# Kernel tuning notes

Hardware: AMD Instinct MI355X
Metric: run time of the kernel (lower is better)

The kernel has to match this reference:

```python
import jax, jax.numpy as jnp
import numpy as np

N, L, H, D = 4, 1024, 8, 64

def setup_inputs() -> dict:
    key = jax.random.key(0)
    ks = jax.random.split(key, 6)
    names = ["q_real", "q_imag", "k_real", "k_imag", "v_real", "v_imag"]
    return {n: jax.random.normal(k, (N, L, H, D), dtype=jnp.float32) for n, k in zip(names, ks)}


def reference(q_real, q_imag, k_real, k_imag, v_real, v_imag):
    d = q_real.shape[-1]
    scale = 1.0 / np.sqrt(d).astype(np.float32)
    # complex QK^T: (ar+i*ai)(br+i*bi) -> 4 real einsums, scores shape (N,H,L,S)
    s_real = (jnp.einsum('nlhd,nshd->nhls', q_real, k_real)
              - jnp.einsum('nlhd,nshd->nhls', q_imag, k_imag))
    s_imag = (jnp.einsum('nlhd,nshd->nhls', q_real, k_imag)
              + jnp.einsum('nlhd,nshd->nhls', q_imag, k_real))
    # complex softmax = independent softmax on real and imag parts
    w_real = jax.nn.softmax(scale * s_real, axis=-1)
    w_imag = jax.nn.softmax(scale * s_imag, axis=-1)
    # complex_dropout on complex input is identity (original code drops nothing)
    # complex AV
    u_real = (jnp.einsum('nhls,nshd->nlhd', w_real, v_real)
              - jnp.einsum('nhls,nshd->nlhd', w_imag, v_imag))
    u_imag = (jnp.einsum('nhls,nshd->nlhd', w_real, v_imag)
              + jnp.einsum('nhls,nshd->nlhd', w_imag, v_real))
    # attn_weights.permute(0,2,1,3).mean(dim=-2): (N,H,L,S)->(N,L,H,S), mean over H -> (N,L,S)
    a_real = w_real.mean(axis=1)
    a_imag = w_imag.mean(axis=1)
    return (u_real, u_imag, a_real, a_imag)
```

## Files before the change

kernel.cpp:

```cpp
#include <hip/hip_runtime.h>

#define N_ 4
#define L_ 1024
#define H_ 8
#define D_ 64

typedef _Float16 f16x8 __attribute__((ext_vector_type(8)));
typedef _Float16 f16x4 __attribute__((ext_vector_type(4)));
typedef _Float16 f16x2 __attribute__((ext_vector_type(2)));
typedef float f32x4 __attribute__((ext_vector_type(4)));

#define MFMA(A, B, C) __builtin_amdgcn_mfma_f32_16x16x32_f16(A, B, C, 0, 0, 0)

__device__ __forceinline__ ushort f2h(float x) {
    union { _Float16 h; ushort u; } c;
    c.h = (_Float16)x;
    return c.u;
}
__device__ __forceinline__ f16x8 ld8(const ushort* p) {
    return *(const f16x8*)p;
}
__device__ __forceinline__ f16x4 pack4(float a, float b, float c, float d) {
    union { f16x4 v; f16x2 h[2]; } u;
    u.h[0] = __builtin_bit_cast(f16x2, __builtin_amdgcn_cvt_pkrtz(a, b));
    u.h[1] = __builtin_bit_cast(f16x2, __builtin_amdgcn_cvt_pkrtz(c, d));
    return u.v;
}
__device__ __forceinline__ f16x8 negf(f16x8 a) {
    uint4 u = __builtin_bit_cast(uint4, a);
    u.x ^= 0x80008000u; u.y ^= 0x80008000u; u.z ^= 0x80008000u; u.w ^= 0x80008000u;
    return __builtin_bit_cast(f16x8, u);
}
__device__ __forceinline__ f16x8 cvt8s(const float* p, float s) {
    float4 a = *(const float4*)p;
    float4 b = *(const float4*)(p + 4);
    union { f16x8 v; _Float16 e[8]; } u;
    u.e[0] = (_Float16)(a.x * s); u.e[1] = (_Float16)(a.y * s);
    u.e[2] = (_Float16)(a.z * s); u.e[3] = (_Float16)(a.w * s);
    u.e[4] = (_Float16)(b.x * s); u.e[5] = (_Float16)(b.y * s);
    u.e[6] = (_Float16)(b.z * s); u.e[7] = (_Float16)(b.w * s);
    return u.v;
}
#define SCQ 0.18033688011112f
__device__ __forceinline__ f16x8 cvt8(const float* p) { return cvt8s(p, SCQ); }

__device__ __forceinline__ void gl_lds16(const ushort* g, ushort* l) {
    __builtin_amdgcn_global_load_lds(
        (const __attribute__((address_space(1))) unsigned int*)g,
        (__attribute__((address_space(3))) unsigned int*)l, 16, 0, 0);
}

__global__ void cvt_k(const float* __restrict__ k_r, const float* __restrict__ k_i,
                      ushort* __restrict__ dst) {
    int gid = blockIdx.x * 256 + threadIdx.x;
    int aid = gid >> 19;
    int idx = (gid & 0x7FFFF) << 2;
    int d  = idx & 63;
    int l  = (idx >> 6) & 1023;
    int hh = (idx >> 16) & 7;
    int n  = idx >> 19;
    const float* src = aid ? k_i : k_r;
    const float4 v = *(const float4*)(src + (((long)n * 1024 + l) * 8 + hh) * 64 + d);
    ushort4 o = make_ushort4(f2h(v.x), f2h(v.y), f2h(v.z), f2h(v.w));
    *(ushort4*)(dst + ((long)aid << 21) + idx) = o;
}

__global__ void cvt_v(const float* __restrict__ vr, const float* __restrict__ vi,
                      ushort* __restrict__ dst) {
    __shared__ ushort t[64][72];
    int bid = blockIdx.x;
    int aid = bid >> 9;
    int b   = bid & 511;
    int s0  = (b & 15) << 6;
    int hh  = (b >> 4) & 7;
    int n   = b >> 7;
    const float* src = aid ? vi : vr;
    int tid = threadIdx.x;
    int r  = tid >> 4;
    int cq = (tid & 15) << 2;
#pragma unroll
    for (int it = 0; it < 4; ++it) {
        int s = s0 + it * 16 + r;
        const float4 v = *(const float4*)(src + (((long)n * 1024 + s) * 8 + hh) * 64 + cq);
        t[it * 16 + r][cq + 0] = f2h(v.x);
        t[it * 16 + r][cq + 1] = f2h(v.y);
        t[it * 16 + r][cq + 2] = f2h(v.z);
        t[it * 16 + r][cq + 3] = f2h(v.w);
    }
    __syncthreads();
    const int rem = cq & 31;
    const int noff = (cq & 32) + (((rem & 15) >> 2) << 3) + ((rem >> 4) << 2);
#pragma unroll
    for (int it = 0; it < 4; ++it) {
        int dd = it * 16 + r;
        ushort4 o;
        o.x = t[cq + 0][dd]; o.y = t[cq + 1][dd]; o.z = t[cq + 2][dd]; o.w = t[cq + 3][dd];
        *(ushort4*)(dst + ((long)aid << 21) + (((long)n * 8 + hh) * 64 + dd) * 1024 + s0 + noff) = o;
    }
}


__launch_bounds__(512, 4)
__global__ void attn_u(const float* __restrict__ qr_g, const float* __restrict__ qi_g,
                       const ushort* __restrict__ ws, float* __restrict__ rdbuf,
                       float* __restrict__ out) {
    __shared__ ushort stgK[2][4096];
    __shared__ ushort stgV[2][4096];

    const int tid  = threadIdx.x;
    const int lane = tid & 63;
    const int wv   = tid >> 6;
    const int p    = wv >> 2;
    const int lsub = wv & 3;
    const int col  = lane & 15;
    const int g    = lane >> 4;

    const int id = blockIdx.x;
    const int x  = id & 7;
    const int j  = id >> 3;
    const int nh = x * 4 + (j >> 4);
    const int n  = nh >> 3;
    const int h  = nh & 7;
    const int l0 = (j & 15) * 64 + lsub * 16;

    const ushort* Kr = ws + ((long)nh << 16);
    const ushort* Ki = ws + (1l << 21) + ((long)nh << 16);
    const ushort* Vr = ws + (2l << 21) + ((long)nh << 16);
    const ushort* Vi = ws + (3l << 21) + ((long)nh << 16);

    const long qg = (((long)n * 1024 + l0 + col) * 8 + h) * 64 + g * 8;
    const float sgn = p ? SCQ : -SCQ;
    const f16x8 qr0 = cvt8(qr_g + qg), qr1 = cvt8(qr_g + qg + 32);
    const f16x8 qx0 = cvt8s(qi_g + qg, sgn), qx1 = cvt8s(qi_g + qg + 32, sgn);

    const int kpart = tid >> 8;
    const int ksr   = (tid >> 3) & 31;
    const int kbo   = (tid & 7) ^ (ksr & 7);
    const ushort* Ksrc = (kpart ? Ki : Kr);
    const int vd  = tid >> 3;
    const int vb  = (tid & 7) ^ (vd & 7);
    const ushort* Vsrc = ((vb >> 2) ? Vi : Vr);
    const int vbo = (vb & 3) * 8;
    ushort* kdst0 = &stgK[0][wv * 512];
    ushort* kdst1 = &stgK[1][wv * 512];
    ushort* vdst0 = &stgV[0][wv * 512];
    ushort* vdst1 = &stgV[1][wv * 512];

    float dsum = 0.f;
    f32x4 uA[4], uB[4];
#pragma unroll
    for (int db = 0; db < 4; ++db) {
        uA[db] = (f32x4){0.f, 0.f, 0.f, 0.f};
        uB[db] = (f32x4){0.f, 0.f, 0.f, 0.f};
    }

    const int kx  = (g ^ (col & 7)) * 8;
    const int kx2 = ((g + 4) ^ (col & 7)) * 8;
    const int vxA = (g ^ (col & 7)) * 8;
    const int vxB = ((4 + g) ^ (col & 7)) * 8;

#define STAGE(kd, vd_, cc)                                                   \
    do {                                                                     \
        gl_lds16(Ksrc + (long)((cc) * 32 + ksr) * 64 + kbo * 8, kd);         \
        gl_lds16(Vsrc + (long)vd * 1024 + (cc) * 32 + vbo, vd_);             \
    } while (0)

    STAGE(kdst0, vdst0, 0);
    __syncthreads();

    for (int cc = 0; cc < 32; ++cc) {
        const int buf = cc & 1;
        if (cc < 31) {
            if (buf) STAGE(kdst0, vdst0, cc + 1);
            else     STAGE(kdst1, vdst1, cc + 1);
        }
        const ushort* sk = stgK[buf];
        const ushort* sv = stgV[buf];

        union { f16x8 w8; f16x4 q[2]; } pw;
#pragma unroll
        for (int sb = 0; sb < 2; ++sb) {
            const int rb = (sb * 16 + col) * 64;
            f16x8 ka0 = ld8(&sk[p * 2048 + rb + kx]);
            f16x8 ka1 = ld8(&sk[p * 2048 + rb + kx2]);
            f16x8 kb0 = ld8(&sk[(p ^ 1) * 2048 + rb + kx]);
            f16x8 kb1 = ld8(&sk[(p ^ 1) * 2048 + rb + kx2]);
            f32x4 a0 = (f32x4){0.f, 0.f, 0.f, 0.f};
            a0 = MFMA(ka0, qr0, a0); a0 = MFMA(ka1, qr1, a0);
            a0 = MFMA(kb0, qx0, a0); a0 = MFMA(kb1, qx1, a0);
            const float w0 = exp2f(a0[0]), w1 = exp2f(a0[1]);
            const float w2 = exp2f(a0[2]), w3 = exp2f(a0[3]);
            dsum += (w0 + w1) + (w2 + w3);
            pw.q[sb] = pack4(w0, w1, w2, w3);
        }

        __builtin_amdgcn_s_setprio(1);
#pragma unroll
        for (int db = 0; db < 4; ++db) {
            const int rv = (db * 16 + col) * 64;
            uA[db] = MFMA(pw.w8, ld8(&sv[rv + vxA]), uA[db]);
            uB[db] = MFMA(pw.w8, ld8(&sv[rv + vxB]), uB[db]);
        }
        __builtin_amdgcn_s_setprio(0);

        __syncthreads();
    }

    dsum += __shfl_xor(dsum, 16);
    dsum += __shfl_xor(dsum, 32);
    const float rd = 1.f / dsum;
    if (lane < 16) rdbuf[p * 32768 + nh * 1024 + l0 + col] = rd;

    float rdl[4];
#pragma unroll
    for (int r = 0; r < 4; ++r) rdl[r] = __shfl(rd, 4 * g + r);

#pragma unroll
    for (int db = 0; db < 4; ++db) {
#pragma unroll
        for (int r = 0; r < 4; ++r) {
            uA[db][r] *= rdl[r];
            uB[db][r] *= rdl[r];
        }
    }

    float* cb = (float*)&stgK[0][0];
    const int ci = (lsub * 64 + lane) * 16;
    if (p == 1) {
#pragma unroll
        for (int db = 0; db < 4; ++db) *(f32x4*)&cb[ci + db * 4] = uB[db];
    }
    __syncthreads();
    f32x4 oR[4];
    if (p == 0) {
#pragma unroll
        for (int db = 0; db < 4; ++db) oR[db] = uA[db] - *(f32x4*)&cb[ci + db * 4];
    }
    __syncthreads();
    if (p == 1) {
#pragma unroll
        for (int db = 0; db < 4; ++db) *(f32x4*)&cb[ci + db * 4] = uA[db];
    }
    __syncthreads();

    if (p == 0) {
        const long OFF_UI = 2097152;
#pragma unroll
        for (int db = 0; db < 4; ++db) {
            f32x4 oI = uB[db] + *(f32x4*)&cb[ci + db * 4];
#pragma unroll
            for (int r = 0; r < 4; ++r) {
                const int l = l0 + 4 * g + r;
                const int d = db * 16 + col;
                const long base = (((long)n * L_ + l) * H_ + h) * D_ + d;
                out[base] = oR[db][r];
                out[OFF_UI + base] = oI[r];
            }
        }
    }
#undef STAGE
}

__launch_bounds__(256, 4)
__global__ void kern_a(const float* __restrict__ qr_g, const float* __restrict__ qi_g,
                      const ushort* __restrict__ ws, const float* __restrict__ rdbuf,
                      float* __restrict__ out) {
    __shared__ ushort stgK[2][2][64][64];
    __shared__ float lrd[8][2][64];

    const int tid  = threadIdx.x;
    const int lane = tid & 63;
    const int wv   = tid >> 6;
    const int col  = lane & 15;
    const int g    = lane >> 4;

    const int id  = blockIdx.x;
    const int x   = id & 7;
    const int q   = id >> 3;
    const int n   = x >> 1;
    const int idx = (x & 1) * 128 + q;
    const int lt0 = (idx >> 4) * 64;
    const int sc  = idx & 15;
    const int l0  = lt0 + wv * 16;

    const ushort* KrB = ws + ((long)(n * 8) << 16);
    const ushort* KiB = ws + (1l << 21) + ((long)(n * 8) << 16);

#pragma unroll
    for (int i = 0; i < 4; ++i) {
        const int t = i * 256 + tid;
        (&lrd[0][0][0])[t] =
            rdbuf[((t >> 6) & 1) * 32768 + (n * 8 + (t >> 7)) * 1024 + lt0 + (t & 63)];
    }

    const int sp   = wv >> 1;
    const int kbs  = ((lane & 7) ^ (lane >> 3)) * 8;

#define STAGEA(buf, hh)                                                      \
    do {                                                                     \
        const ushort* Kp = (sp ? KiB : KrB) + ((long)(hh) << 16);            \
        _Pragma("unroll")                                                    \
        for (int i = 0; i < 4; ++i) {                                        \
            const int krow = (wv & 1) * 32 + i * 8 + (lane >> 3);            \
            gl_lds16(Kp + (long)(sc * 64 + krow) * 64 + kbs,                 \
                     &stgK[buf][sp][(wv & 1) * 32 + i * 8][0]);              \
        }                                                                    \
    } while (0)

    f32x4 aR[4], aI[4];
#pragma unroll
    for (int i = 0; i < 4; ++i) {
        aR[i] = (f32x4){0.f, 0.f, 0.f, 0.f};
        aI[i] = (f32x4){0.f, 0.f, 0.f, 0.f};
    }

    const int kx  = (g ^ (col & 7)) * 8;
    const int kx2 = ((g + 4) ^ (col & 7)) * 8;

    STAGEA(0, 0);
    __syncthreads();

    for (int h = 0; h < 8; ++h) {
        const int buf = h & 1;
        if (h < 7) STAGEA(buf ^ 1, h + 1);

        const long qg = (((long)n * 1024 + l0 + col) * 8 + h) * 64 + g * 8;
        const f16x8 qr0 = cvt8(qr_g + qg), qr1 = cvt8(qr_g + qg + 32);
        const f16x8 qi0 = cvt8(qi_g + qg), qi1 = cvt8(qi_g + qg + 32);
        const f16x8 qn0 = negf(qi0), qn1 = negf(qi1);

        float rdR[4], rdI[4];
#pragma unroll
        for (int r = 0; r < 4; ++r) {
            rdR[r] = lrd[h][0][wv * 16 + 4 * g + r];
            rdI[r] = lrd[h][1][wv * 16 + 4 * g + r];
        }

#pragma unroll
        for (int sb = 0; sb < 4; ++sb) {
            const int row = sb * 16 + col;
            f16x8 kr0 = ld8(&stgK[buf][0][row][kx]);
            f16x8 kr1 = ld8(&stgK[buf][0][row][kx2]);
            f16x8 ki0 = ld8(&stgK[buf][1][row][kx]);
            f16x8 ki1 = ld8(&stgK[buf][1][row][kx2]);
            f32x4 a0 = (f32x4){0.f, 0.f, 0.f, 0.f};
            a0 = MFMA(qr0, kr0, a0); a0 = MFMA(qr1, kr1, a0);
            a0 = MFMA(qn0, ki0, a0); a0 = MFMA(qn1, ki1, a0);
            f32x4 a1 = (f32x4){0.f, 0.f, 0.f, 0.f};
            a1 = MFMA(qr0, ki0, a1); a1 = MFMA(qr1, ki1, a1);
            a1 = MFMA(qi0, kr0, a1); a1 = MFMA(qi1, kr1, a1);
#pragma unroll
            for (int r = 0; r < 4; ++r) {
                aR[sb][r] += exp2f(a0[r]) * rdR[r];
                aI[sb][r] += exp2f(a1[r]) * rdI[r];
            }
        }
        __syncthreads();
    }

    const long OFF_AR = 4194304;
    const long OFF_AI = 8388608;
#pragma unroll
    for (int sb = 0; sb < 4; ++sb) {
#pragma unroll
        for (int r = 0; r < 4; ++r) {
            const int l = l0 + 4 * g + r;
            const int s = sc * 64 + sb * 16 + col;
            const long ab = ((long)n * 1024 + l) * 1024 + s;
            out[OFF_AR + ab] = aR[sb][r] * 0.125f;
            out[OFF_AI + ab] = aI[sb][r] * 0.125f;
        }
    }
#undef STAGEA
}

extern "C" void kernel_launch(void* const* d_in, const int* in_sizes, int n_in,
                              void* d_out, int out_size, void* d_ws, size_t ws_size,
                              hipStream_t stream) {
    const float* qr = (const float*)d_in[0];
    const float* qi = (const float*)d_in[1];
    const float* kr = (const float*)d_in[2];
    const float* ki = (const float*)d_in[3];
    const float* vr = (const float*)d_in[4];
    const float* vi = (const float*)d_in[5];
    ushort* ws = (ushort*)d_ws;
    float* rdbuf = (float*)((char*)d_ws + (16ull << 20));
    float* out = (float*)d_out;

    hipLaunchKernelGGL(cvt_k, dim3(4096), dim3(256), 0, stream, kr, ki, ws);
    hipLaunchKernelGGL(cvt_v, dim3(1024), dim3(256), 0, stream, vr, vi, ws + (2l << 21));
    hipLaunchKernelGGL(attn_u, dim3(512), dim3(512), 0, stream, qr, qi, ws, rdbuf, out);
    hipLaunchKernelGGL(kern_a, dim3(1024), dim3(256), 0, stream, qr, qi, ws, rdbuf, out);
}
```

Baseline: 103.9 us.

## Compute both real and imaginary softmax per wave and triple-buffer K/V staging

Each wave now computes both the real and imaginary score tiles and all four complex AV accumulators for its 16 query rows, instead of splitting real/imag across two wave groups. This removes the cross-wave LDS reduction at the end and doubles the work reused per staged K/V chunk, halving the grid to 256 blocks of 128 rows. The staging moves from double to triple buffering with explicit vmcnt waits and raw barriers, so loads run two chunks ahead. In exchange, register use per wave roughly doubles, launch bounds drop to 2 blocks per CU, and there are fewer blocks to fill the GPU.

```diff
diff --git a/kernel.cpp b/kernel.cpp
--- a/kernel.cpp
+++ b/kernel.cpp
@@ -100,28 +100,26 @@
 }
 
 
-__launch_bounds__(512, 4)
+__launch_bounds__(512, 2)
 __global__ void attn_u(const float* __restrict__ qr_g, const float* __restrict__ qi_g,
                        const ushort* __restrict__ ws, float* __restrict__ rdbuf,
                        float* __restrict__ out) {
-    __shared__ ushort stgK[2][4096];
-    __shared__ ushort stgV[2][4096];
+    __shared__ ushort stgK[3][4096];
+    __shared__ ushort stgV[3][4096];
 
     const int tid  = threadIdx.x;
     const int lane = tid & 63;
     const int wv   = tid >> 6;
-    const int p    = wv >> 2;
-    const int lsub = wv & 3;
     const int col  = lane & 15;
     const int g    = lane >> 4;
 
     const int id = blockIdx.x;
     const int x  = id & 7;
     const int j  = id >> 3;
-    const int nh = x * 4 + (j >> 4);
+    const int nh = x * 4 + (j >> 3);
     const int n  = nh >> 3;
     const int h  = nh & 7;
-    const int l0 = (j & 15) * 64 + lsub * 16;
+    const int l0 = (j & 7) * 128 + wv * 16;
 
     const ushort* Kr = ws + ((long)nh << 16);
     const ushort* Ki = ws + (1l << 21) + ((long)nh << 16);
@@ -129,9 +127,9 @@
     const ushort* Vi = ws + (3l << 21) + ((long)nh << 16);
 
     const long qg = (((long)n * 1024 + l0 + col) * 8 + h) * 64 + g * 8;
-    const float sgn = p ? SCQ : -SCQ;
     const f16x8 qr0 = cvt8(qr_g + qg), qr1 = cvt8(qr_g + qg + 32);
-    const f16x8 qx0 = cvt8s(qi_g + qg, sgn), qx1 = cvt8s(qi_g + qg + 32, sgn);
+    const f16x8 qn0 = cvt8s(qi_g + qg, -SCQ), qn1 = cvt8s(qi_g + qg + 32, -SCQ);
+    const f16x8 qp0 = negf(qn0), qp1 = negf(qn1);
 
     const int kpart = tid >> 8;
     const int ksr   = (tid >> 3) & 31;
@@ -141,17 +139,15 @@
     const int vb  = (tid & 7) ^ (vd & 7);
     const ushort* Vsrc = ((vb >> 2) ? Vi : Vr);
     const int vbo = (vb & 3) * 8;
-    ushort* kdst0 = &stgK[0][wv * 512];
-    ushort* kdst1 = &stgK[1][wv * 512];
-    ushort* vdst0 = &stgV[0][wv * 512];
-    ushort* vdst1 = &stgV[1][wv * 512];
-
-    float dsum = 0.f;
-    f32x4 uA[4], uB[4];
+
+    float dsR = 0.f, dsI = 0.f;
+    f32x4 uRR[4], uII[4], uRI[4], uIR[4];
 #pragma unroll
     for (int db = 0; db < 4; ++db) {
-        uA[db] = (f32x4){0.f, 0.f, 0.f, 0.f};
-        uB[db] = (f32x4){0.f, 0.f, 0.f, 0.f};
+        uRR[db] = (f32x4){0.f, 0.f, 0.f, 0.f};
+        uII[db] = (f32x4){0.f, 0.f, 0.f, 0.f};
+        uRI[db] = (f32x4){0.f, 0.f, 0.f, 0.f};
+        uIR[db] = (f32x4){0.f, 0.f, 0.f, 0.f};
     }
 
     const int kx  = (g ^ (col & 7)) * 8;
@@ -159,103 +155,97 @@
     const int vxA = (g ^ (col & 7)) * 8;
     const int vxB = ((4 + g) ^ (col & 7)) * 8;
 
-#define STAGE(kd, vd_, cc)                                                   \
+#define STAGE(bb, cc)                                                        \
     do {                                                                     \
-        gl_lds16(Ksrc + (long)((cc) * 32 + ksr) * 64 + kbo * 8, kd);         \
-        gl_lds16(Vsrc + (long)vd * 1024 + (cc) * 32 + vbo, vd_);             \
+        gl_lds16(Ksrc + (long)((cc) * 32 + ksr) * 64 + kbo * 8,              \
+                 &stgK[bb][wv * 512]);                                       \
+        gl_lds16(Vsrc + (long)vd * 1024 + (cc) * 32 + vbo,                   \
+                 &stgV[bb][wv * 512]);                                       \
     } while (0)
 
-    STAGE(kdst0, vdst0, 0);
-    __syncthreads();
-
+    STAGE(0, 0);
+    STAGE(1, 1);
+    asm volatile("s_waitcnt vmcnt(2)" ::: "memory");
+    __builtin_amdgcn_s_barrier();
+
+    int bc = 0, bp = 2;
     for (int cc = 0; cc < 32; ++cc) {
-        const int buf = cc & 1;
-        if (cc < 31) {
-            if (buf) STAGE(kdst0, vdst0, cc + 1);
-            else     STAGE(kdst1, vdst1, cc + 1);
-        }
-        const ushort* sk = stgK[buf];
-        const ushort* sv = stgV[buf];
-
-        union { f16x8 w8; f16x4 q[2]; } pw;
+        if (cc < 30) STAGE(bp, cc + 2);
+        const ushort* sk = &stgK[bc][0];
+        const ushort* sv = &stgV[bc][0];
+
+        union { f16x8 w8; f16x4 q[2]; } pw0, pw1;
 #pragma unroll
         for (int sb = 0; sb < 2; ++sb) {
             const int rb = (sb * 16 + col) * 64;
-            f16x8 ka0 = ld8(&sk[p * 2048 + rb + kx]);
-            f16x8 ka1 = ld8(&sk[p * 2048 + rb + kx2]);
-            f16x8 kb0 = ld8(&sk[(p ^ 1) * 2048 + rb + kx]);
-            f16x8 kb1 = ld8(&sk[(p ^ 1) * 2048 + rb + kx2]);
+            f16x8 kr0 = ld8(&sk[rb + kx]);
+            f16x8 kr1 = ld8(&sk[rb + kx2]);
+            f16x8 ki0 = ld8(&sk[2048 + rb + kx]);
+            f16x8 ki1 = ld8(&sk[2048 + rb + kx2]);
             f32x4 a0 = (f32x4){0.f, 0.f, 0.f, 0.f};
-            a0 = MFMA(ka0, qr0, a0); a0 = MFMA(ka1, qr1, a0);
-            a0 = MFMA(kb0, qx0, a0); a0 = MFMA(kb1, qx1, a0);
+            a0 = MFMA(kr0, qr0, a0); a0 = MFMA(kr1, qr1, a0);
+            a0 = MFMA(ki0, qn0, a0); a0 = MFMA(ki1, qn1, a0);
+            f32x4 a1 = (f32x4){0.f, 0.f, 0.f, 0.f};
+            a1 = MFMA(ki0, qr0, a1); a1 = MFMA(ki1, qr1, a1);
+            a1 = MFMA(kr0, qp0, a1); a1 = MFMA(kr1, qp1, a1);
             const float w0 = exp2f(a0[0]), w1 = exp2f(a0[1]);
             const float w2 = exp2f(a0[2]), w3 = exp2f(a0[3]);
-            dsum += (w0 + w1) + (w2 + w3);
-            pw.q[sb] = pack4(w0, w1, w2, w3);
+            dsR += (w0 + w1) + (w2 + w3);
+            pw0.q[sb] = pack4(w0, w1, w2, w3);
+            const float v0 = exp2f(a1[0]), v1 = exp2f(a1[1]);
+            const float v2 = exp2f(a1[2]), v3 = exp2f(a1[3]);
+            dsI += (v0 + v1) + (v2 + v3);
+            pw1.q[sb] = pack4(v0, v1, v2, v3);
         }
 
         __builtin_amdgcn_s_setprio(1);
 #pragma unroll
         for (int db = 0; db < 4; ++db) {
             const int rv = (db * 16 + col) * 64;
-            uA[db] = MFMA(pw.w8, ld8(&sv[rv + vxA]), uA[db]);
-            uB[db] = MFMA(pw.w8, ld8(&sv[rv + vxB]), uB[db]);
+            f16x8 vA = ld8(&sv[rv + vxA]);
+            f16x8 vB = ld8(&sv[rv + vxB]);
+            uRR[db] = MFMA(pw0.w8, vA, uRR[db]);
+            uIR[db] = MFMA(pw1.w8, vA, uIR[db]);
+            uRI[db] = MFMA(pw0.w8, vB, uRI[db]);
+            uII[db] = MFMA(pw1.w8, vB, uII[db]);
         }
         __builtin_amdgcn_s_setprio(0);
 
-        __syncthreads();
-    }
-
-    dsum += __shfl_xor(dsum, 16);
-    dsum += __shfl_xor(dsum, 32);
-    const float rd = 1.f / dsum;
-    if (lane < 16) rdbuf[p * 32768 + nh * 1024 + l0 + col] = rd;
-
-    float rdl[4];
-#pragma unroll
-    for (int r = 0; r < 4; ++r) rdl[r] = __shfl(rd, 4 * g + r);
-
+        if (cc < 31) {
+            if (cc < 30) asm volatile("s_waitcnt vmcnt(2)" ::: "memory");
+            else         asm volatile("s_waitcnt vmcnt(0)" ::: "memory");
+            __builtin_amdgcn_s_barrier();
+        }
+        bc = (bc == 2) ? 0 : bc + 1;
+        bp = (bp == 2) ? 0 : bp + 1;
+    }
+
+    dsR += __shfl_xor(dsR, 16); dsR += __shfl_xor(dsR, 32);
+    dsI += __shfl_xor(dsI, 16); dsI += __shfl_xor(dsI, 32);
+    const float rdR = 1.f / dsR;
+    const float rdI = 1.f / dsI;
+    if (lane < 16) {
+        rdbuf[nh * 1024 + l0 + col] = rdR;
+        rdbuf[32768 + nh * 1024 + l0 + col] = rdI;
+    }
+
+    float rlR[4], rlI[4];
+#pragma unroll
+    for (int r = 0; r < 4; ++r) {
+        rlR[r] = __shfl(rdR, 4 * g + r);
+        rlI[r] = __shfl(rdI, 4 * g + r);
+    }
+
+    const long OFF_UI = 2097152;
 #pragma unroll
     for (int db = 0; db < 4; ++db) {
 #pragma unroll
         for (int r = 0; r < 4; ++r) {
-            uA[db][r] *= rdl[r];
-            uB[db][r] *= rdl[r];
-        }
-    }
-
-    float* cb = (float*)&stgK[0][0];
-    const int ci = (lsub * 64 + lane) * 16;
-    if (p == 1) {
-#pragma unroll
-        for (int db = 0; db < 4; ++db) *(f32x4*)&cb[ci + db * 4] = uB[db];
-    }
-    __syncthreads();
-    f32x4 oR[4];
-    if (p == 0) {
-#pragma unroll
-        for (int db = 0; db < 4; ++db) oR[db] = uA[db] - *(f32x4*)&cb[ci + db * 4];
-    }
-    __syncthreads();
-    if (p == 1) {
-#pragma unroll
-        for (int db = 0; db < 4; ++db) *(f32x4*)&cb[ci + db * 4] = uA[db];
-    }
-    __syncthreads();
-
-    if (p == 0) {
-        const long OFF_UI = 2097152;
-#pragma unroll
-        for (int db = 0; db < 4; ++db) {
-            f32x4 oI = uB[db] + *(f32x4*)&cb[ci + db * 4];
-#pragma unroll
-            for (int r = 0; r < 4; ++r) {
-                const int l = l0 + 4 * g + r;
-                const int d = db * 16 + col;
-                const long base = (((long)n * L_ + l) * H_ + h) * D_ + d;
-                out[base] = oR[db][r];
-                out[OFF_UI + base] = oI[r];
-            }
+            const int l = l0 + 4 * g + r;
+            const int d = db * 16 + col;
+            const long base = (((long)n * L_ + l) * H_ + h) * D_ + d;
+            out[base] = uRR[db][r] * rlR[r] - uII[db][r] * rlI[r];
+            out[OFF_UI + base] = uRI[db][r] * rlR[r] + uIR[db][r] * rlI[r];
         }
     }
 #undef STAGE
@@ -389,6 +379,6 @@
 
     hipLaunchKernelGGL(cvt_k, dim3(4096), dim3(256), 0, stream, kr, ki, ws);
     hipLaunchKernelGGL(cvt_v, dim3(1024), dim3(256), 0, stream, vr, vi, ws + (2l << 21));
-    hipLaunchKernelGGL(attn_u, dim3(512), dim3(512), 0, stream, qr, qi, ws, rdbuf, out);
+    hipLaunchKernelGGL(attn_u, dim3(256), dim3(512), 0, stream, qr, qi, ws, rdbuf, out);
     hipLaunchKernelGGL(kern_a, dim3(1024), dim3(256), 0, stream, qr, qi, ws, rdbuf, out);
 }
```

Result: no change. 105.8 us (+1.9%).
